# Optimization experiments

Hardware: AMD Instinct MI355X
Metric: run time of the kernel (lower is better)

## Reference

```python
import jax, jax.numpy as jnp
import numpy as np

EPS = 1e-5
W_LOSS = 1.0


def setup_inputs() -> dict:
    key = jax.random.key(0)
    k1, k2 = jax.random.split(key)
    heatmap = jax.random.uniform(k1, (128, 98, 64, 64), dtype=jnp.float32)
    groundtruth = jax.random.uniform(k2, (128, 98, 2), dtype=jnp.float32)
    return {"heatmap": heatmap, "groundtruth": groundtruth}


def _grid(h, w, dtype):
    # torch.meshgrid(arange(h), arange(w)) 'ij' convention: yy[i,j]=y(i), xx[i,j]=x(j)
    ys = (jnp.arange(h, dtype=dtype) / (h - 1)) * 2.0 - 1.0
    xs = (jnp.arange(w, dtype=dtype) / (w - 1)) * 2.0 - 1.0
    yy = jnp.broadcast_to(ys[:, None], (h, w))
    xx = jnp.broadcast_to(xs[None, :], (h, w))
    return yy, xx


def reference(heatmap, groundtruth):
    b, n, h, w = heatmap.shape
    # normalize heatmap to a distribution per (b, n)
    hm = heatmap / jnp.clip(heatmap.sum((2, 3)), 1e-6)[:, :, None, None]
    yy, xx = _grid(h, w, hm.dtype)
    # weighted mean -> soft-argmax coords (x, y)
    mx = (hm * xx[None, None]).sum((2, 3))  # [b, n]
    my = (hm * yy[None, None]).sum((2, 3))  # [b, n]
    means = jnp.stack([mx, my], axis=-1)    # [b, n, 2]
    # unbiased weighted covariance
    dx = xx[None, None] - mx[:, :, None, None]           # [b, n, h, w]
    dy = yy[None, None] - my[:, :, None, None]           # [b, n, h, w]
    d = jnp.stack([dx, dy], axis=2).reshape(b, n, 2, h * w)  # [b, n, 2, hw]
    wv = hm.reshape(b, n, 1, h * w)
    cov = jnp.einsum('bnih,bnjh->bnij', wv * d, d)        # [b, n, 2, 2]
    V1 = hm.sum((2, 3)) + EPS
    V2 = (hm * hm).sum((2, 3)) + EPS
    denom = V1 - V2 / V1
    cov = cov / denom[:, :, None, None]
    # symmetric eig (ascending eigenvalues, columns are eigenvectors),
    # same convention as torch.symeig(eigenvectors=True)
    evals, evecs = jnp.linalg.eigh(cov)                   # [b,n,2], [b,n,2,2]
    # ambiguity guided decompose: pts (1x2) @ V^T
    pts = groundtruth - means                             # [b, n, 2]
    rotate = jnp.einsum('bni,bnji->bnj', pts, evecs)      # [b, n, 2]
    scale = rotate / jnp.sqrt(evals + EPS)
    # dist='l2' -> F.mse_loss(zeros, scale)
    loss_trans = jnp.mean(scale * scale)
    loss_eigen = jnp.mean(jnp.abs(evals).sum(-1))
    return loss_trans + W_LOSS * loss_eigen
```

## Files before the change

### kernel.cpp

```cpp
#include <hip/hip_runtime.h>

#define EPSF 1e-5f

__global__ __launch_bounds__(256) void star_pair_kernel(
    const float* __restrict__ heatmap,
    const float* __restrict__ gt,
    float* __restrict__ pair_out)
{
    const int pair = blockIdx.x;
    const float* hp = heatmap + (size_t)pair * 4096;
    const int t = threadIdx.x;

    const float cgrid = 2.0f / 63.0f;

    float s0 = 0.f, s1 = 0.f, s2 = 0.f, s3 = 0.f, s4 = 0.f, s5 = 0.f, s6 = 0.f;

    #pragma unroll
    for (int i = 0; i < 4; ++i) {
        const int f = t + i * 256;
        const float4 v = reinterpret_cast<const float4*>(hp)[f];
        const int y = f >> 4;
        const int x0 = (f & 15) << 2;
        const float yf = fmaf((float)y, cgrid, -1.0f);
        const float a[4] = {v.x, v.y, v.z, v.w};
        #pragma unroll
        for (int k = 0; k < 4; ++k) {
            const float xf = fmaf((float)(x0 + k), cgrid, -1.0f);
            const float av = a[k];
            s0 += av;
            s6 = fmaf(av, av, s6);
            s1 = fmaf(av, xf, s1);
            s2 = fmaf(av, yf, s2);
            const float ax = av * xf;
            s3 = fmaf(ax, xf, s3);
            s4 = fmaf(ax, yf, s4);
            const float ay = av * yf;
            s5 = fmaf(ay, yf, s5);
        }
    }

    #pragma unroll
    for (int off = 32; off >= 1; off >>= 1) {
        s0 += __shfl_down(s0, off);
        s1 += __shfl_down(s1, off);
        s2 += __shfl_down(s2, off);
        s3 += __shfl_down(s3, off);
        s4 += __shfl_down(s4, off);
        s5 += __shfl_down(s5, off);
        s6 += __shfl_down(s6, off);
    }

    __shared__ float red[4][7];
    const int wave = t >> 6;
    const int lane = t & 63;
    if (lane == 0) {
        red[wave][0] = s0; red[wave][1] = s1; red[wave][2] = s2;
        red[wave][3] = s3; red[wave][4] = s4; red[wave][5] = s5;
        red[wave][6] = s6;
    }
    __syncthreads();

    if (t == 0) {
        s0 = red[0][0] + red[1][0] + red[2][0] + red[3][0];
        s1 = red[0][1] + red[1][1] + red[2][1] + red[3][1];
        s2 = red[0][2] + red[1][2] + red[2][2] + red[3][2];
        s3 = red[0][3] + red[1][3] + red[2][3] + red[3][3];
        s4 = red[0][4] + red[1][4] + red[2][4] + red[3][4];
        s5 = red[0][5] + red[1][5] + red[2][5] + red[3][5];
        s6 = red[0][6] + red[1][6] + red[2][6] + red[3][6];

        const float S = s0 > 1e-6f ? s0 : 1e-6f;
        const float inv = 1.0f / S;
        const float T  = s0 * inv;
        const float mx = s1 * inv;
        const float my = s2 * inv;
        const float Exx = s3 * inv;
        const float Exy = s4 * inv;
        const float Eyy = s5 * inv;
        const float V2raw = s6 * inv * inv;

        const float c2mT = 2.0f - T;
        float c00 = Exx - mx * mx * c2mT;
        float c01 = Exy - mx * my * c2mT;
        float c11 = Eyy - my * my * c2mT;
        const float V1 = T + EPSF;
        const float denom = V1 - (V2raw + EPSF) / V1;
        const float idn = 1.0f / denom;
        c00 *= idn; c01 *= idn; c11 *= idn;

        const float mmid = 0.5f * (c00 + c11);
        const float h = 0.5f * (c00 - c11);
        const float r = sqrtf(h * h + c01 * c01);
        const float l0 = mmid - r;
        const float l1 = mmid + r;
        float vx = h + r, vy = c01;
        const float nn = vx * vx + vy * vy;
        float cc, ssn;
        if (nn > 1e-30f) {
            const float rin = rsqrtf(nn);
            cc = vx * rin; ssn = vy * rin;
        } else {
            cc = 0.0f; ssn = 1.0f;
        }

        const float px = gt[2 * pair]     - mx;
        const float py = gt[2 * pair + 1] - my;
        const float r1 = cc * px + ssn * py;
        const float r0 = -ssn * px + cc * py;

        const float ssum = r0 * r0 / (l0 + EPSF) + r1 * r1 / (l1 + EPSF);
        const float esum = fabsf(l0) + fabsf(l1);
        pair_out[pair] = 0.5f * ssum + esum;
    }
}

__global__ __launch_bounds__(1024) void star_reduce_kernel(
    const float* __restrict__ pair_out,
    float* __restrict__ out,
    int n, float inv_n)
{
    float s = 0.f;
    for (int i = threadIdx.x; i < n; i += 1024) s += pair_out[i];
    #pragma unroll
    for (int off = 32; off >= 1; off >>= 1) s += __shfl_down(s, off);
    __shared__ float red[16];
    const int wave = threadIdx.x >> 6;
    const int lane = threadIdx.x & 63;
    if (lane == 0) red[wave] = s;
    __syncthreads();
    if (threadIdx.x == 0) {
        float tot = 0.f;
        #pragma unroll
        for (int w = 0; w < 16; ++w) tot += red[w];
        out[0] = tot * inv_n;
    }
}

extern "C" void kernel_launch(void* const* d_in, const int* in_sizes, int n_in,
                              void* d_out, int out_size, void* d_ws, size_t ws_size,
                              hipStream_t stream) {
    const float* heatmap = (const float*)d_in[0];
    const float* gt      = (const float*)d_in[1];
    float* out = (float*)d_out;
    float* pair_out = (float*)d_ws;

    const int npairs = in_sizes[1] / 2;

    star_pair_kernel<<<npairs, 256, 0, stream>>>(heatmap, gt, pair_out);
    star_reduce_kernel<<<1, 1024, 0, stream>>>(pair_out, out, npairs,
                                               1.0f / (float)npairs);
}
```

Before: 277.1 us.

## Map one wavefront per heatmap pair instead of one block per pair

Each 256-thread block now processes four pairs, one per wavefront, and each lane handles 16 float4 loads of its pair. The x-grid coordinates are hoisted per lane. The cross-wave shared-memory reduction and __syncthreads are removed, since each pair is reduced purely with wave shuffles. This gives more memory-level parallelism per thread and less sync overhead, at the cost of a longer per-thread serial accumulation and fewer blocks.

```diff
diff --git a/kernel.cpp b/kernel.cpp
--- a/kernel.cpp
+++ b/kernel.cpp
@@ -5,38 +5,52 @@
 __global__ __launch_bounds__(256) void star_pair_kernel(
     const float* __restrict__ heatmap,
     const float* __restrict__ gt,
-    float* __restrict__ pair_out)
+    float* __restrict__ pair_out,
+    int npairs)
 {
-    const int pair = blockIdx.x;
+    const int t = threadIdx.x;
+    const int wave = t >> 6;
+    const int lane = t & 63;
+    const int pair = blockIdx.x * 4 + wave;
+    if (pair >= npairs) return;
+
     const float* hp = heatmap + (size_t)pair * 4096;
-    const int t = threadIdx.x;
 
     const float cgrid = 2.0f / 63.0f;
+    const float xb = (float)((lane & 15) << 2);
+    const float xf0 = fmaf(xb,          cgrid, -1.0f);
+    const float xf1 = fmaf(xb + 1.0f,   cgrid, -1.0f);
+    const float xf2 = fmaf(xb + 2.0f,   cgrid, -1.0f);
+    const float xf3 = fmaf(xb + 3.0f,   cgrid, -1.0f);
+    const int   yb  = lane >> 4;
 
     float s0 = 0.f, s1 = 0.f, s2 = 0.f, s3 = 0.f, s4 = 0.f, s5 = 0.f, s6 = 0.f;
 
     #pragma unroll
-    for (int i = 0; i < 4; ++i) {
-        const int f = t + i * 256;
-        const float4 v = reinterpret_cast<const float4*>(hp)[f];
-        const int y = f >> 4;
-        const int x0 = (f & 15) << 2;
-        const float yf = fmaf((float)y, cgrid, -1.0f);
-        const float a[4] = {v.x, v.y, v.z, v.w};
-        #pragma unroll
-        for (int k = 0; k < 4; ++k) {
-            const float xf = fmaf((float)(x0 + k), cgrid, -1.0f);
-            const float av = a[k];
-            s0 += av;
-            s6 = fmaf(av, av, s6);
-            s1 = fmaf(av, xf, s1);
-            s2 = fmaf(av, yf, s2);
-            const float ax = av * xf;
-            s3 = fmaf(ax, xf, s3);
-            s4 = fmaf(ax, yf, s4);
-            const float ay = av * yf;
-            s5 = fmaf(ay, yf, s5);
-        }
+    for (int j = 0; j < 16; ++j) {
+        const float4 v = reinterpret_cast<const float4*>(hp)[lane + (j << 6)];
+        const float yf = fmaf((float)(yb + (j << 2)), cgrid, -1.0f);
+        const float a0 = v.x, a1 = v.y, a2 = v.z, a3 = v.w;
+
+        s0 += a0; s6 = fmaf(a0, a0, s6);
+        s1 = fmaf(a0, xf0, s1); s2 = fmaf(a0, yf, s2);
+        { const float ax = a0 * xf0; s3 = fmaf(ax, xf0, s3); s4 = fmaf(ax, yf, s4); }
+        { const float ay = a0 * yf;  s5 = fmaf(ay, yf, s5); }
+
+        s0 += a1; s6 = fmaf(a1, a1, s6);
+        s1 = fmaf(a1, xf1, s1); s2 = fmaf(a1, yf, s2);
+        { const float ax = a1 * xf1; s3 = fmaf(ax, xf1, s3); s4 = fmaf(ax, yf, s4); }
+        { const float ay = a1 * yf;  s5 = fmaf(ay, yf, s5); }
+
+        s0 += a2; s6 = fmaf(a2, a2, s6);
+        s1 = fmaf(a2, xf2, s1); s2 = fmaf(a2, yf, s2);
+        { const float ax = a2 * xf2; s3 = fmaf(ax, xf2, s3); s4 = fmaf(ax, yf, s4); }
+        { const float ay = a2 * yf;  s5 = fmaf(ay, yf, s5); }
+
+        s0 += a3; s6 = fmaf(a3, a3, s6);
+        s1 = fmaf(a3, xf3, s1); s2 = fmaf(a3, yf, s2);
+        { const float ax = a3 * xf3; s3 = fmaf(ax, xf3, s3); s4 = fmaf(ax, yf, s4); }
+        { const float ay = a3 * yf;  s5 = fmaf(ay, yf, s5); }
     }
 
     #pragma unroll
@@ -50,25 +64,7 @@
         s6 += __shfl_down(s6, off);
     }
 
-    __shared__ float red[4][7];
-    const int wave = t >> 6;
-    const int lane = t & 63;
     if (lane == 0) {
-        red[wave][0] = s0; red[wave][1] = s1; red[wave][2] = s2;
-        red[wave][3] = s3; red[wave][4] = s4; red[wave][5] = s5;
-        red[wave][6] = s6;
-    }
-    __syncthreads();
-
-    if (t == 0) {
-        s0 = red[0][0] + red[1][0] + red[2][0] + red[3][0];
-        s1 = red[0][1] + red[1][1] + red[2][1] + red[3][1];
-        s2 = red[0][2] + red[1][2] + red[2][2] + red[3][2];
-        s3 = red[0][3] + red[1][3] + red[2][3] + red[3][3];
-        s4 = red[0][4] + red[1][4] + red[2][4] + red[3][4];
-        s5 = red[0][5] + red[1][5] + red[2][5] + red[3][5];
-        s6 = red[0][6] + red[1][6] + red[2][6] + red[3][6];
-
         const float S = s0 > 1e-6f ? s0 : 1e-6f;
         const float inv = 1.0f / S;
         const float T  = s0 * inv;
@@ -145,8 +141,9 @@
     float* pair_out = (float*)d_ws;
 
     const int npairs = in_sizes[1] / 2;
+    const int nblocks = (npairs + 3) / 4;
 
-    star_pair_kernel<<<npairs, 256, 0, stream>>>(heatmap, gt, pair_out);
+    star_pair_kernel<<<nblocks, 256, 0, stream>>>(heatmap, gt, pair_out, npairs);
     star_reduce_kernel<<<1, 1024, 0, stream>>>(pair_out, out, npairs,
                                                1.0f / (float)npairs);
 }
```

After: 280.7 us. About the same (+1.3%).
